# Performance work log

Hardware: AMD Instinct MI355X
Metric: run time of the kernel (lower is better)

The kernel has to match this reference:

```python
import jax, jax.numpy as jnp
import numpy as np

DIM = 768
HEADS = 12
DIM_HEAD = 64
INNER = HEADS * DIM_HEAD  # 768
EPS = 1e-5


def setup_inputs() -> dict:
    key = jax.random.key(0)
    ks = jax.random.split(key, 5)
    x = jax.random.normal(ks[0], (4, 2048, DIM), dtype=jnp.float32)
    ln_g = jnp.ones((DIM,), dtype=jnp.float32)
    ln_b = jnp.zeros((DIM,), dtype=jnp.float32)
    s1 = 1.0 / np.sqrt(DIM)
    W_qkv = jax.random.uniform(ks[1], (DIM, 3 * INNER), dtype=jnp.float32, minval=-s1, maxval=s1)
    b_qkv = jax.random.uniform(ks[2], (3 * INNER,), dtype=jnp.float32, minval=-s1, maxval=s1)
    s2 = 1.0 / np.sqrt(INNER)
    W_out = jax.random.uniform(ks[3], (INNER, DIM), dtype=jnp.float32, minval=-s2, maxval=s2)
    b_out = jax.random.uniform(ks[4], (DIM,), dtype=jnp.float32, minval=-s2, maxval=s2)
    return {"x": x, "ln_g": ln_g, "ln_b": ln_b, "W_qkv": W_qkv, "b_qkv": b_qkv, "W_out": W_out, "b_out": b_out}


def reference(x, ln_g, ln_b, W_qkv, b_qkv, W_out, b_out):
    b, n, _ = x.shape
    # pre-norm LayerNorm
    mu = jnp.mean(x, axis=-1, keepdims=True)
    var = jnp.mean(jnp.square(x - mu), axis=-1, keepdims=True)
    xn = (x - mu) * jax.lax.rsqrt(var + EPS) * ln_g + ln_b
    qkv = xn @ W_qkv + b_qkv  # [b, n, 3*inner]
    q, k, v = jnp.split(qkv, 3, axis=-1)
    def to_heads(t):
        return t.reshape(b, n, HEADS, DIM_HEAD).transpose(0, 2, 1, 3)  # b h n d
    q, k, v = map(to_heads, (q, k, v))
    q = q * (DIM_HEAD ** -0.5)
    sim = jnp.einsum('bhid,bhjd->bhij', q, k)
    attn = jax.nn.softmax(sim, axis=-1)  # dropout is identity (p=0.0)
    out = jnp.einsum('bhij,bhjd->bhid', attn, v)
    out = out.transpose(0, 2, 1, 3).reshape(b, n, INNER)
    return out @ W_out + b_out
```

## Files before the change

### kernel.cpp

```cpp
#include <hip/hip_runtime.h>
#include <cstdint>
#include <cstddef>


#define SEQ    2048
#define NBATCH 4
#define DMODEL 768
#define NHEADS 12
#define DHEAD  64
#define MROWS  (NBATCH * SEQ)
#define NQKV   (3 * DMODEL)
#define KT     64
#define NT     (SEQ / KT)

using f32x4  = __attribute__((ext_vector_type(4))) float;
using u16x8  = __attribute__((ext_vector_type(8))) unsigned short;
using s16x8  = __attribute__((ext_vector_type(8))) short;
using u16x4  = __attribute__((ext_vector_type(4))) unsigned short;
using s16x4  = __attribute__((ext_vector_type(4))) short;

__device__ __forceinline__ unsigned short f2bf(float f) {
  union { float f; unsigned int u; } x; x.f = f;
  unsigned int r = x.u + 0x7fffu + ((x.u >> 16) & 1u);
  return (unsigned short)(r >> 16);
}

#if defined(__has_builtin)
#if __has_builtin(__builtin_amdgcn_cvt_pk_bf16_f32)
#define HAVE_PK_BF16 1
#endif
#if __has_builtin(__builtin_amdgcn_exp2f)
#define HAVE_EXP2 1
#endif
#if __has_builtin(__builtin_amdgcn_mfma_f32_16x16x16bf16_1k)
#define HAVE_MFMA_16X16X16_BF16 1
#endif
#endif

__device__ __forceinline__ unsigned int pk_bf16(float a, float b) {
#ifdef HAVE_PK_BF16
  auto v = __builtin_amdgcn_cvt_pk_bf16_f32(a, b);
  union { decltype(v) v2; unsigned int u; } c; c.v2 = v; return c.u;
#else
  return (unsigned int)f2bf(a) | ((unsigned int)f2bf(b) << 16);
#endif
}

__device__ __forceinline__ float fexp2(float x) {
#ifdef HAVE_EXP2
  return __builtin_amdgcn_exp2f(x);
#else
  return exp2f(x);
#endif
}

__device__ __forceinline__ f32x4 mfma16(u16x8 a, u16x8 b, f32x4 c) {
  return __builtin_amdgcn_mfma_f32_16x16x32_bf16((s16x8)a, (s16x8)b, c, 0, 0, 0);
}

__device__ __forceinline__ f32x4 mfma16k16(u16x4 a, u16x4 b, f32x4 c) {
#ifdef HAVE_MFMA_16X16X16_BF16
  return __builtin_amdgcn_mfma_f32_16x16x16bf16_1k((s16x4)a, (s16x4)b, c, 0, 0, 0);
#else
  f32x4 d;
  asm("v_mfma_f32_16x16x16_bf16 %0, %1, %2, %3"
      : "=v"(d) : "v"(a), "v"(b), "v"(c));
  return d;
#endif
}

__device__ __forceinline__ void gl_lds16(const void* g, void* l) {
  __builtin_amdgcn_global_load_lds(
      (const __attribute__((address_space(1))) void*)g,
      (__attribute__((address_space(3))) void*)l, 16, 0, 0);
}

__global__ __launch_bounds__(256) void lntconv_kernel(
    const float* __restrict__ x, const float* __restrict__ g,
    const float* __restrict__ bb, unsigned short* __restrict__ xn,
    const float* __restrict__ Wq, const float* __restrict__ Wo,
    unsigned short* __restrict__ Wqt, unsigned short* __restrict__ Wot) {
  __shared__ float tile[32][33];
  const int t = threadIdx.x;
  int id = blockIdx.x;
  if (id < 2048) {
    const int wid = t >> 6, l = t & 63;
    const int row = id * 4 + wid;
    const float4* xr = (const float4*)(x + (size_t)row * DMODEL);
    float4 xa = xr[l], xb2 = xr[64 + l], xc = xr[128 + l];
    float s = (xa.x + xa.y) + (xa.z + xa.w) + (xb2.x + xb2.y) + (xb2.z + xb2.w)
            + (xc.x + xc.y) + (xc.z + xc.w);
    float q = xa.x * xa.x + xa.y * xa.y + xa.z * xa.z + xa.w * xa.w
            + xb2.x * xb2.x + xb2.y * xb2.y + xb2.z * xb2.z + xb2.w * xb2.w
            + xc.x * xc.x + xc.y * xc.y + xc.z * xc.z + xc.w * xc.w;
#pragma unroll
    for (int o = 32; o; o >>= 1) { s += __shfl_xor(s, o); q += __shfl_xor(q, o); }
    const float mu = s * (1.0f / DMODEL);
    const float var = q * (1.0f / DMODEL) - mu * mu;
    const float rstd = rsqrtf(var + 1e-5f);
    const float4* gp = (const float4*)g;
    const float4* bp = (const float4*)bb;
    uint2* dst = (uint2*)(xn + (size_t)row * DMODEL);
#pragma unroll
    for (int c = 0; c < 3; ++c) {
      float4 xv = (c == 0) ? xa : (c == 1) ? xb2 : xc;
      float4 gv = gp[c * 64 + l], bv = bp[c * 64 + l];
      float y0 = (xv.x - mu) * rstd * gv.x + bv.x;
      float y1 = (xv.y - mu) * rstd * gv.y + bv.y;
      float y2 = (xv.z - mu) * rstd * gv.z + bv.z;
      float y3 = (xv.w - mu) * rstd * gv.w + bv.w;
      uint2 pk; pk.x = pk_bf16(y0, y1); pk.y = pk_bf16(y2, y3);
      dst[c * 64 + l] = pk;
    }
    return;
  }
  id -= 2048;
  const float* W; unsigned short* Wt; int N, n0, k0;
  if (id < 1728) { W = Wq; Wt = Wqt; N = NQKV;   n0 = (id % 72) * 32; k0 = (id / 72) * 32; }
  else { id -= 1728; W = Wo; Wt = Wot; N = DMODEL; n0 = (id % 24) * 32; k0 = (id / 24) * 32; }
  const int tx = t & 31, ty = t >> 5;
#pragma unroll
  for (int r = 0; r < 4; ++r)
    tile[ty + r * 8][tx] = W[(size_t)(k0 + ty + r * 8) * N + n0 + tx];
  __syncthreads();
#pragma unroll
  for (int r = 0; r < 4; ++r)
    Wt[(size_t)(n0 + ty + r * 8) * DMODEL + k0 + tx] = f2bf(tile[tx][ty + r * 8]);
}

__global__ __launch_bounds__(256, 3) void gemm_qkv_kernel(
    const unsigned short* __restrict__ Wt, const unsigned short* __restrict__ xn,
    const float* __restrict__ bias, unsigned short* __restrict__ qb,
    unsigned short* __restrict__ kb, unsigned short* __restrict__ vt) {
  __shared__ alignas(16) unsigned short As[128 * 64];
  __shared__ alignas(16) unsigned short Bs[128 * 64];
  const int t = threadIdx.x, wid = t >> 6, l = t & 63, quad = l >> 4, ll = l & 15;
  const int bid = blockIdx.x;
  const int w = (bid & 7) * 96 + (bid >> 3);
  const int srow = l >> 3, sblk = (l & 7) ^ srow;

  const int wq = w % 12;
  const int a0 = wq * 128;
  const int b0 = (w / 12) * 128;
  const int m0 = b0 + (wq & 1) * 64;
  const int n0 = 2 * DMODEL + (wq >> 1) * 128;
  const unsigned short* A2 = xn + (size_t)m0 * DMODEL;
  const unsigned short* B2 = Wt + (size_t)n0 * DMODEL;

  auto stage2 = [&](int k0) {
#pragma unroll
    for (int cc = 0; cc < 2; ++cc) {
      int call = wid * 2 + cc;
      int r = call * 8 + srow;
      gl_lds16(A2 + (size_t)r * DMODEL + k0 + sblk * 8, &As[call * 512]);
    }
#pragma unroll
    for (int cc = 0; cc < 4; ++cc) {
      int call = wid * 4 + cc;
      int r = call * 8 + srow;
      gl_lds16(B2 + (size_t)r * DMODEL + k0 + sblk * 8, &Bs[call * 512]);
    }
  };

  {
    const unsigned short* Ap = Wt + (size_t)a0 * DMODEL;
    const unsigned short* Bp = xn + (size_t)b0 * DMODEL;
    const int wa = (wid >> 1) * 64, wb = (wid & 1) * 64;
    f32x4 acc[4][4] = {};
    for (int k0 = 0; k0 < DMODEL; k0 += 64) {
#pragma unroll
      for (int cc = 0; cc < 4; ++cc) {
        int call = wid * 4 + cc;
        int r = call * 8 + srow;
        gl_lds16(Ap + (size_t)r * DMODEL + k0 + sblk * 8, &As[call * 512]);
        gl_lds16(Bp + (size_t)r * DMODEL + k0 + sblk * 8, &Bs[call * 512]);
      }
      __syncthreads();
#pragma unroll
      for (int ks = 0; ks < 2; ++ks) {
        u16x8 af[4], bf[4];
#pragma unroll
        for (int i = 0; i < 4; ++i) {
          int ra = wa + i * 16 + ll, rb = wb + i * 16 + ll;
          int blk = (ks * 4 + quad) ^ (ll & 7);
          af[i] = *(const u16x8*)&As[ra * 64 + blk * 8];
          bf[i] = *(const u16x8*)&Bs[rb * 64 + blk * 8];
        }
#pragma unroll
        for (int mi = 0; mi < 4; ++mi)
#pragma unroll
          for (int ni = 0; ni < 4; ++ni)
            acc[mi][ni] = mfma16(af[mi], bf[ni], acc[mi][ni]);
      }
      __syncthreads();
    }
    stage2(0);
    const bool isq = (a0 < DMODEL);
    unsigned short* dst = isq ? qb : kb;
    const float sc = isq ? 0.18033688f : 1.0f;
#pragma unroll
    for (int mi = 0; mi < 4; ++mi) {
      int row0 = a0 + wa + mi * 16 + quad * 4;
      float4 bv = *(const float4*)&bias[row0];
      int rr = isq ? row0 : row0 - DMODEL;
      int h = rr >> 6, d0 = rr & 63;
#pragma unroll
      for (int ni = 0; ni < 4; ++ni) {
        int seq = b0 + wb + ni * 16 + ll;
        int b = seq >> 11, i = seq & 2047;
        uint2 pk;
        pk.x = pk_bf16((acc[mi][ni][0] + bv.x) * sc, (acc[mi][ni][1] + bv.y) * sc);
        pk.y = pk_bf16((acc[mi][ni][2] + bv.z) * sc, (acc[mi][ni][3] + bv.w) * sc);
        *(uint2*)&dst[(size_t)((b * NHEADS + h) * SEQ + i) * DHEAD + d0] = pk;
      }
    }
  }

  {
    const int wm = (wid >> 1) * 32, wn = (wid & 1) * 64;
    f32x4 acc[2][4] = {};
    for (int k0 = 0; k0 < DMODEL; k0 += 64) {
      __syncthreads();
#pragma unroll
      for (int ks = 0; ks < 2; ++ks) {
        u16x8 af[2], bf[4];
#pragma unroll
        for (int i = 0; i < 2; ++i) {
          int ra = wm + i * 16 + ll;
          int blk = (ks * 4 + quad) ^ (ll & 7);
          af[i] = *(const u16x8*)&As[ra * 64 + blk * 8];
        }
#pragma unroll
        for (int i = 0; i < 4; ++i) {
          int rb = wn + i * 16 + ll;
          int blk = (ks * 4 + quad) ^ (ll & 7);
          bf[i] = *(const u16x8*)&Bs[rb * 64 + blk * 8];
        }
#pragma unroll
        for (int mi = 0; mi < 2; ++mi)
#pragma unroll
          for (int ni = 0; ni < 4; ++ni)
            acc[mi][ni] = mfma16(af[mi], bf[ni], acc[mi][ni]);
      }
      if (k0 + 64 < DMODEL) {
        __syncthreads();
        stage2(k0 + 64);
      }
    }
#pragma unroll
    for (int mi = 0; mi < 2; ++mi) {
      int gm = m0 + wm + mi * 16 + quad * 4;
      int b = gm >> 11, i0 = gm & 2047;
#pragma unroll
      for (int ni = 0; ni < 4; ++ni) {
        int gn = n0 + wn + ni * 16 + ll;
        float bv = bias[gn];
        int rem = gn - 2 * DMODEL;
        int h = rem >> 6, d = rem & 63;
        int bh = b * NHEADS + h;
        uint2 pk;
        pk.x = pk_bf16(acc[mi][ni][0] + bv, acc[mi][ni][1] + bv);
        pk.y = pk_bf16(acc[mi][ni][2] + bv, acc[mi][ni][3] + bv);
        *(uint2*)&vt[((size_t)bh * DHEAD + d) * SEQ + i0] = pk;
      }
    }
  }
}

__global__ __launch_bounds__(256, 3) void attn_kernel(
    const unsigned short* __restrict__ qbuf, const unsigned short* __restrict__ kbuf,
    const unsigned short* __restrict__ vtg, unsigned short* __restrict__ ao) {
  __shared__ alignas(16) unsigned short stage[3][2][KT * DHEAD];
  const int t = threadIdx.x, wid = t >> 6, l = t & 63, quad = l >> 4, ll = l & 15;
  const int Lid = blockIdx.y * 16 + blockIdx.x;
  const int w = (Lid & 7) * 96 + (Lid >> 3);
  const int qt = w & 15, bh = w >> 4;
  const unsigned short* qg  = qbuf + ((size_t)bh * SEQ + qt * 128) * DHEAD;
  const unsigned short* kg0 = kbuf + (size_t)bh * SEQ * DHEAD;
  const unsigned short* vt0 = vtg  + (size_t)bh * DHEAD * SEQ;
  const int srow = l >> 3;
  const int sblk = (l & 7) ^ srow;

  unsigned short* Qs = &stage[0][0][0];
#pragma unroll
  for (int cc = 0; cc < 4; ++cc) {
    int call = wid * 4 + cc;
    gl_lds16(qg + (call * 8 + srow) * 64 + sblk * 8, Qs + call * 512);
  }
  __syncthreads();
  u16x8 qf[2][2];
#pragma unroll
  for (int mi = 0; mi < 2; ++mi)
#pragma unroll
    for (int ks = 0; ks < 2; ++ks) {
      int r = wid * 32 + mi * 16 + ll;
      int blk = (ks * 4 + quad) ^ (ll & 7);
      qf[mi][ks] = *(const u16x8*)&Qs[r * 64 + blk * 8];
    }
  __syncthreads();

  auto stage_tile = [&](int buf, int kt2) {
    const unsigned short* kg = kg0 + (size_t)kt2 * KT * DHEAD;
#pragma unroll
    for (int c = 0; c < 2; ++c) {
      int call = wid * 2 + c;
      int r = call * 8 + srow;
      gl_lds16(kg + r * 64 + sblk * 8, &stage[buf][0][call * 512]);
      gl_lds16(vt0 + (size_t)r * SEQ + kt2 * KT + sblk * 8, &stage[buf][1][call * 512]);
    }
  };

  f32x4 oacc[2][4] = {};
  f32x4 osum[2] = {};
  const u16x4 onesb = {0x3f80u, 0x3f80u, 0x3f80u, 0x3f80u};

  stage_tile(0, 0);
  stage_tile(1, 1);
  int bufc = 0, bufs = 2;
  for (int kt2 = 0; kt2 < NT; ++kt2) {
    if (kt2 + 1 < NT) asm volatile("s_waitcnt vmcnt(4)" ::: "memory");
    else              asm volatile("s_waitcnt vmcnt(0)" ::: "memory");
    __builtin_amdgcn_s_barrier();
    if (kt2 + 2 < NT) stage_tile(bufs, kt2 + 2);
    const unsigned short* Ks = &stage[bufc][0][0];
    const unsigned short* Vs = &stage[bufc][1][0];

    f32x4 st[2][4] = {};
    __builtin_amdgcn_s_setprio(1);
#pragma unroll
    for (int ks = 0; ks < 2; ++ks)
#pragma unroll
      for (int ni = 0; ni < 4; ++ni) {
        int r = ni * 16 + ll;
        int blk = (ks * 4 + quad) ^ (ll & 7);
        u16x8 kf = *(const u16x8*)&Ks[r * 64 + blk * 8];
        st[0][ni] = mfma16(kf, qf[0][ks], st[0][ni]);
        st[1][ni] = mfma16(kf, qf[1][ks], st[1][ni]);
      }
    __builtin_amdgcn_s_setprio(0);

#pragma unroll
    for (int ni = 0; ni < 4; ++ni) {
      u16x4 pf[2];
#pragma unroll
      for (int mi = 0; mi < 2; ++mi) {
        float p0 = fexp2(st[mi][ni][0]);
        float p1 = fexp2(st[mi][ni][1]);
        float p2 = fexp2(st[mi][ni][2]);
        float p3 = fexp2(st[mi][ni][3]);
        union { uint2 u; u16x4 v; } cv;
        cv.u.x = pk_bf16(p0, p1);
        cv.u.y = pk_bf16(p2, p3);
        pf[mi] = cv.v;
      }
      const int voff = (((ni * 2 + (quad >> 1)) ^ (ll & 7)) << 3) + (quad & 1) * 4;
      __builtin_amdgcn_s_setprio(1);
      osum[0] = mfma16k16(pf[0], onesb, osum[0]);
      osum[1] = mfma16k16(pf[1], onesb, osum[1]);
#pragma unroll
      for (int di = 0; di < 4; ++di) {
        u16x4 vf = *(const u16x4*)&Vs[(di * 16 + ll) * 64 + voff];
        oacc[0][di] = mfma16k16(pf[0], vf, oacc[0][di]);
        oacc[1][di] = mfma16k16(pf[1], vf, oacc[1][di]);
      }
      __builtin_amdgcn_s_setprio(0);
    }
    bufc = (bufc == 2) ? 0 : bufc + 1;
    bufs = (bufs == 2) ? 0 : bufs + 1;
  }

  const int b = bh / NHEADS, h = bh - b * NHEADS;
#pragma unroll
  for (int mi = 0; mi < 2; ++mi) {
#pragma unroll
    for (int r = 0; r < 4; ++r) {
      float inv = 1.0f / osum[mi][r];
      int row = qt * 128 + wid * 32 + mi * 16 + quad * 4 + r;
      size_t base = ((size_t)(b * SEQ + row)) * DMODEL + h * DHEAD;
#pragma unroll
      for (int di = 0; di < 4; ++di)
        ao[base + di * 16 + ll] = f2bf(oacc[mi][di][r] * inv);
    }
  }
}

__global__ __launch_bounds__(256, 3) void gemm_out_kernel(
    const unsigned short* __restrict__ Wt, const unsigned short* __restrict__ ao,
    const float* __restrict__ bias, float* __restrict__ out) {
  __shared__ alignas(16) unsigned short As[64 * 64];
  __shared__ alignas(16) unsigned short Bs[128 * 64];
  const int t = threadIdx.x, wid = t >> 6, l = t & 63, quad = l >> 4, ll = l & 15;
  const int bid = blockIdx.x;
  const int w = (bid & 7) * 96 + (bid >> 3);
  const int a0 = (w % 12) * 64;
  const int b0 = (w / 12) * 128;
  const int wa = (wid >> 1) * 32, wb = (wid & 1) * 64;
  const int srow = l >> 3, sblk = (l & 7) ^ srow;
  f32x4 acc[2][4] = {};
  for (int k0 = 0; k0 < DMODEL; k0 += 64) {
#pragma unroll
    for (int cc = 0; cc < 6; ++cc) {
      int call = wid * 6 + cc;
      if (call < 8) {
        int r = call * 8 + srow;
        gl_lds16(Wt + (size_t)(a0 + r) * DMODEL + k0 + sblk * 8, &As[call * 512]);
      } else {
        int c2 = call - 8;
        int r = c2 * 8 + srow;
        gl_lds16(ao + (size_t)(b0 + r) * DMODEL + k0 + sblk * 8, &Bs[c2 * 512]);
      }
    }
    __syncthreads();
#pragma unroll
    for (int ks = 0; ks < 2; ++ks) {
      u16x8 af[2], bf[4];
#pragma unroll
      for (int i = 0; i < 2; ++i) {
        int ra = wa + i * 16 + ll;
        int blk = (ks * 4 + quad) ^ (ll & 7);
        af[i] = *(const u16x8*)&As[ra * 64 + blk * 8];
      }
#pragma unroll
      for (int i = 0; i < 4; ++i) {
        int rb = wb + i * 16 + ll;
        int blk = (ks * 4 + quad) ^ (ll & 7);
        bf[i] = *(const u16x8*)&Bs[rb * 64 + blk * 8];
      }
#pragma unroll
      for (int mi = 0; mi < 2; ++mi)
#pragma unroll
        for (int ni = 0; ni < 4; ++ni)
          acc[mi][ni] = mfma16(af[mi], bf[ni], acc[mi][ni]);
    }
    __syncthreads();
  }
#pragma unroll
  for (int mi = 0; mi < 2; ++mi) {
    int row0 = a0 + wa + mi * 16 + quad * 4;
    float4 bv = *(const float4*)&bias[row0];
#pragma unroll
    for (int ni = 0; ni < 4; ++ni) {
      int seq = b0 + wb + ni * 16 + ll;
      float4 o;
      o.x = acc[mi][ni][0] + bv.x;
      o.y = acc[mi][ni][1] + bv.y;
      o.z = acc[mi][ni][2] + bv.z;
      o.w = acc[mi][ni][3] + bv.w;
      *(float4*)&out[(size_t)seq * DMODEL + row0] = o;
    }
  }
}

extern "C" void kernel_launch(void* const* d_in, const int* in_sizes, int n_in,
                              void* d_out, int out_size, void* d_ws, size_t ws_size,
                              hipStream_t stream) {
  const float* x     = (const float*)d_in[0];
  const float* ln_g  = (const float*)d_in[1];
  const float* ln_b  = (const float*)d_in[2];
  const float* W_qkv = (const float*)d_in[3];
  const float* b_qkv = (const float*)d_in[4];
  const float* W_out = (const float*)d_in[5];
  const float* b_out = (const float*)d_in[6];
  float* out = (float*)d_out;

  char* ws = (char*)d_ws;
  unsigned short* xn    = (unsigned short*)(ws);
  unsigned short* wqkvt = (unsigned short*)(ws + 12582912);
  unsigned short* woutt = (unsigned short*)(ws + 16121856);
  unsigned short* qb    = (unsigned short*)(ws + 17301504);
  unsigned short* kb    = (unsigned short*)(ws + 29884416);
  unsigned short* vt    = (unsigned short*)(ws + 42467328);
  unsigned short* ao    = xn;

  lntconv_kernel<<<2048 + 2304, 256, 0, stream>>>(x, ln_g, ln_b, xn,
                                                  W_qkv, W_out, wqkvt, woutt);
  gemm_qkv_kernel<<<768, 256, 0, stream>>>(wqkvt, xn, b_qkv, qb, kb, vt);
  attn_kernel<<<dim3(SEQ / 128, NBATCH * NHEADS), 256, 0, stream>>>(qb, kb, vt, ao);
  gemm_out_kernel<<<768, 256, 0, stream>>>(woutt, ao, b_out, out);
}
```

Measured before the change: 209.0 us.

## Fuse QK and V GEMM loops into one K-loop sharing the activation tile

The QKV GEMM previously ran two sequential K-loops: one for the Q/K 128x128 tile and another for a 64x128 V tile that reloaded activation rows from global memory. Both now run in a single K-loop that stages a third weight tile (Cs) and reuses the already-loaded activation tile Bs as the V-GEMM A operand. This removes the redundant activation loads and half the loop and barrier overhead. In exchange it adds 16KB of LDS and keeps both accumulator sets live at once, which raises register pressure and can lower occupancy under launch_bounds(256,3).

```diff
diff --git a/kernel.cpp b/kernel.cpp
--- a/kernel.cpp
+++ b/kernel.cpp
@@ -134,6 +134,7 @@
     unsigned short* __restrict__ kb, unsigned short* __restrict__ vt) {
   __shared__ alignas(16) unsigned short As[128 * 64];
   __shared__ alignas(16) unsigned short Bs[128 * 64];
+  __shared__ alignas(16) unsigned short Cs[128 * 64];
   const int t = threadIdx.x, wid = t >> 6, l = t & 63, quad = l >> 4, ll = l & 15;
   const int bid = blockIdx.x;
   const int w = (bid & 7) * 96 + (bid >> 3);
@@ -142,47 +143,39 @@
   const int wq = w % 12;
   const int a0 = wq * 128;
   const int b0 = (w / 12) * 128;
-  const int m0 = b0 + (wq & 1) * 64;
+  const int m0loc = (wq & 1) * 64;
+  const int m0 = b0 + m0loc;
   const int n0 = 2 * DMODEL + (wq >> 1) * 128;
-  const unsigned short* A2 = xn + (size_t)m0 * DMODEL;
-  const unsigned short* B2 = Wt + (size_t)n0 * DMODEL;
-
-  auto stage2 = [&](int k0) {
-#pragma unroll
-    for (int cc = 0; cc < 2; ++cc) {
-      int call = wid * 2 + cc;
-      int r = call * 8 + srow;
-      gl_lds16(A2 + (size_t)r * DMODEL + k0 + sblk * 8, &As[call * 512]);
-    }
+
+  const unsigned short* Ap = Wt + (size_t)a0 * DMODEL;
+  const unsigned short* Bp = xn + (size_t)b0 * DMODEL;
+  const unsigned short* Cp = Wt + (size_t)n0 * DMODEL;
+
+  const int wa = (wid >> 1) * 64, wb = (wid & 1) * 64;
+  const int wm = (wid >> 1) * 32, wn = (wid & 1) * 64;
+
+  f32x4 acc[4][4] = {};
+  f32x4 acc2[2][4] = {};
+
+  for (int k0 = 0; k0 < DMODEL; k0 += 64) {
 #pragma unroll
     for (int cc = 0; cc < 4; ++cc) {
       int call = wid * 4 + cc;
       int r = call * 8 + srow;
-      gl_lds16(B2 + (size_t)r * DMODEL + k0 + sblk * 8, &Bs[call * 512]);
-    }
-  };
-
-  {
-    const unsigned short* Ap = Wt + (size_t)a0 * DMODEL;
-    const unsigned short* Bp = xn + (size_t)b0 * DMODEL;
-    const int wa = (wid >> 1) * 64, wb = (wid & 1) * 64;
-    f32x4 acc[4][4] = {};
-    for (int k0 = 0; k0 < DMODEL; k0 += 64) {
-#pragma unroll
-      for (int cc = 0; cc < 4; ++cc) {
-        int call = wid * 4 + cc;
-        int r = call * 8 + srow;
-        gl_lds16(Ap + (size_t)r * DMODEL + k0 + sblk * 8, &As[call * 512]);
-        gl_lds16(Bp + (size_t)r * DMODEL + k0 + sblk * 8, &Bs[call * 512]);
-      }
-      __syncthreads();
-#pragma unroll
-      for (int ks = 0; ks < 2; ++ks) {
+      gl_lds16(Ap + (size_t)r * DMODEL + k0 + sblk * 8, &As[call * 512]);
+      gl_lds16(Bp + (size_t)r * DMODEL + k0 + sblk * 8, &Bs[call * 512]);
+      gl_lds16(Cp + (size_t)r * DMODEL + k0 + sblk * 8, &Cs[call * 512]);
+    }
+    __syncthreads();
+#pragma unroll
+    for (int ks = 0; ks < 2; ++ks) {
+      const int blkbase = ks * 4 + quad;
+      {
         u16x8 af[4], bf[4];
 #pragma unroll
         for (int i = 0; i < 4; ++i) {
           int ra = wa + i * 16 + ll, rb = wb + i * 16 + ll;
-          int blk = (ks * 4 + quad) ^ (ll & 7);
+          int blk = blkbase ^ (ll & 7);
           af[i] = *(const u16x8*)&As[ra * 64 + blk * 8];
           bf[i] = *(const u16x8*)&Bs[rb * 64 + blk * 8];
         }
@@ -192,9 +185,31 @@
           for (int ni = 0; ni < 4; ++ni)
             acc[mi][ni] = mfma16(af[mi], bf[ni], acc[mi][ni]);
       }
-      __syncthreads();
-    }
-    stage2(0);
+      {
+        u16x8 af2[2], bf2[4];
+#pragma unroll
+        for (int i = 0; i < 2; ++i) {
+          int ra = m0loc + wm + i * 16 + ll;
+          int blk = blkbase ^ (ll & 7);
+          af2[i] = *(const u16x8*)&Bs[ra * 64 + blk * 8];
+        }
+#pragma unroll
+        for (int i = 0; i < 4; ++i) {
+          int rb = wn + i * 16 + ll;
+          int blk = blkbase ^ (ll & 7);
+          bf2[i] = *(const u16x8*)&Cs[rb * 64 + blk * 8];
+        }
+#pragma unroll
+        for (int mi = 0; mi < 2; ++mi)
+#pragma unroll
+          for (int ni = 0; ni < 4; ++ni)
+            acc2[mi][ni] = mfma16(af2[mi], bf2[ni], acc2[mi][ni]);
+      }
+    }
+    __syncthreads();
+  }
+
+  {
     const bool isq = (a0 < DMODEL);
     unsigned short* dst = isq ? qb : kb;
     const float sc = isq ? 0.18033688f : 1.0f;
@@ -215,38 +230,7 @@
       }
     }
   }
-
   {
-    const int wm = (wid >> 1) * 32, wn = (wid & 1) * 64;
-    f32x4 acc[2][4] = {};
-    for (int k0 = 0; k0 < DMODEL; k0 += 64) {
-      __syncthreads();
-#pragma unroll
-      for (int ks = 0; ks < 2; ++ks) {
-        u16x8 af[2], bf[4];
-#pragma unroll
-        for (int i = 0; i < 2; ++i) {
-          int ra = wm + i * 16 + ll;
-          int blk = (ks * 4 + quad) ^ (ll & 7);
-          af[i] = *(const u16x8*)&As[ra * 64 + blk * 8];
-        }
-#pragma unroll
-        for (int i = 0; i < 4; ++i) {
-          int rb = wn + i * 16 + ll;
-          int blk = (ks * 4 + quad) ^ (ll & 7);
-          bf[i] = *(const u16x8*)&Bs[rb * 64 + blk * 8];
-        }
-#pragma unroll
-        for (int mi = 0; mi < 2; ++mi)
-#pragma unroll
-          for (int ni = 0; ni < 4; ++ni)
-            acc[mi][ni] = mfma16(af[mi], bf[ni], acc[mi][ni]);
-      }
-      if (k0 + 64 < DMODEL) {
-        __syncthreads();
-        stage2(k0 + 64);
-      }
-    }
 #pragma unroll
     for (int mi = 0; mi < 2; ++mi) {
       int gm = m0 + wm + mi * 16 + quad * 4;
@@ -259,8 +243,8 @@
         int h = rem >> 6, d = rem & 63;
         int bh = b * NHEADS + h;
         uint2 pk;
-        pk.x = pk_bf16(acc[mi][ni][0] + bv, acc[mi][ni][1] + bv);
-        pk.y = pk_bf16(acc[mi][ni][2] + bv, acc[mi][ni][3] + bv);
+        pk.x = pk_bf16(acc2[mi][ni][0] + bv, acc2[mi][ni][1] + bv);
+        pk.y = pk_bf16(acc2[mi][ni][2] + bv, acc2[mi][ni][3] + bv);
         *(uint2*)&vt[((size_t)bh * DHEAD + d) * SEQ + i0] = pk;
       }
     }
```

Measured after the change: 211.7 us. About the same (+1.3%).
